# Performance work log

Measured on AMD Instinct MI355X. Metric: run time of the kernel, lower is better.

## Reference

```python
import jax, jax.numpy as jnp
import numpy as np

N, L, D, V, M = 64, 77, 768, 8, 8   # text batch, context_length, width, visual tokens, visual batch
H, LAYERS, VOCAB, E = 12, 12, 49409, 768
SOV, EOT = 49408, 49407  # splice-point token, end-of-text token


def setup_inputs() -> dict:
    rng = np.random.default_rng(0)
    text = rng.integers(1, 49400, size=(N, L))
    pos_y = rng.integers(1, 11, size=N)                      # splice position per sample
    eot = np.minimum(pos_y + rng.integers(5, 31, size=N), L - V)
    text[np.arange(N), pos_y] = SOV
    text[np.arange(N), eot] = EOT

    key = jax.random.key(0)
    ks = jax.random.split(key, 16)
    attn_std = D ** -0.5
    proj_std = (D ** -0.5) * ((2 * LAYERS) ** -0.5)
    fc_std = (2 * D) ** -0.5
    return {
        'text': jnp.asarray(text, jnp.int32),
        'visual_feature': jax.random.normal(ks[0], (M, V, D), jnp.float32),
        'tok_emb': jax.random.normal(ks[1], (VOCAB, D), jnp.float32) * 0.02,
        'pos_emb': jax.random.normal(ks[2], (L, D), jnp.float32) * 0.01,
        'ln1_w': jnp.ones((LAYERS, D), jnp.float32), 'ln1_b': jnp.zeros((LAYERS, D), jnp.float32),
        'in_w': jax.random.normal(ks[3], (LAYERS, 3 * D, D), jnp.float32) * attn_std,
        'in_b': jnp.zeros((LAYERS, 3 * D), jnp.float32),
        'out_w': jax.random.normal(ks[4], (LAYERS, D, D), jnp.float32) * proj_std,
        'out_b': jnp.zeros((LAYERS, D), jnp.float32),
        'ln2_w': jnp.ones((LAYERS, D), jnp.float32), 'ln2_b': jnp.zeros((LAYERS, D), jnp.float32),
        'fc_w': jax.random.normal(ks[5], (LAYERS, 4 * D, D), jnp.float32) * fc_std,
        'fc_b': jnp.zeros((LAYERS, 4 * D), jnp.float32),
        'pj_w': jax.random.normal(ks[6], (LAYERS, D, 4 * D), jnp.float32) * proj_std,
        'pj_b': jnp.zeros((LAYERS, D), jnp.float32),
        'lnf_w': jnp.ones((D,), jnp.float32), 'lnf_b': jnp.zeros((D,), jnp.float32),
        'text_proj': jax.random.normal(ks[7], (D, E), jnp.float32) * attn_std,
    }


def _layer_norm(x, w, b, eps=1e-5):
    mu = x.mean(-1, keepdims=True)
    var = ((x - mu) ** 2).mean(-1, keepdims=True)
    return (x - mu) * jax.lax.rsqrt(var + eps) * w + b


def reference(text, visual_feature, tok_emb, pos_emb, ln1_w, ln1_b, in_w, in_b,
              out_w, out_b, ln2_w, ln2_b, fc_w, fc_b, pj_w, pj_b, lnf_w, lnf_b, text_proj):
    text = text.astype(jnp.int32)
    pos_y = jnp.argmax(text == SOV, axis=1)        # [N] per-sample splice point
    eot = jnp.argmax(text == EOT, axis=1)          # [N]
    x = tok_emb[text]                              # [N,L,D]
    p = jnp.arange(L)[None, :]                     # [1,L]
    # fused gather replacing the torch.cat double loop:
    # out[p] = x[p] for p<pos_y ; visual[p-pos_y] for pos_y<=p<pos_y+V ; x[p-V+1] after
    src = jnp.clip(jnp.where(p < pos_y[:, None], p, p - V + 1), 0, L - 1)   # [N,L]
    xg = jnp.take_along_axis(x, src[..., None], axis=1)                      # [N,L,D]
    vis_mask = (p >= pos_y[:, None]) & (p < pos_y[:, None] + V)              # [N,L]
    vis_idx = jnp.clip(p - pos_y[:, None], 0, V - 1)                         # [N,L]
    vis = visual_feature[:, vis_idx]                                         # [M,N,L,D]
    h = jnp.where(vis_mask[None, :, :, None], vis, xg[None]) + pos_emb       # [M,N,L,D]
    h = h.reshape(M * N, L, D)

    mask = jnp.triu(jnp.full((L, L), -jnp.inf, jnp.float32), k=1)            # causal
    hd = D // H
    scale = 1.0 / np.sqrt(hd).astype(np.float32)
    for l in range(LAYERS):
        y = _layer_norm(h, ln1_w[l], ln1_b[l])
        qkv = y @ in_w[l].T + in_b[l]                                        # [B,L,3D]
        q, k, v = jnp.split(qkv, 3, axis=-1)
        sp = lambda t: t.reshape(-1, L, H, hd).transpose(0, 2, 1, 3)
        q, k, v = sp(q), sp(k), sp(v)
        att = jax.nn.softmax(jnp.einsum('bhqd,bhkd->bhqk', q, k) * scale + mask, axis=-1)
        o = jnp.einsum('bhqk,bhkd->bhqd', att, v).transpose(0, 2, 1, 3).reshape(-1, L, D)
        h = h + o @ out_w[l].T + out_b[l]
        y = _layer_norm(h, ln2_w[l], ln2_b[l]) @ fc_w[l].T + fc_b[l]
        y = y * jax.nn.sigmoid(1.702 * y)                                    # QuickGELU
        h = h + y @ pj_w[l].T + pj_b[l]

    h = _layer_norm(h, lnf_w, lnf_b).reshape(M, N, L, D)
    feats = h[:, jnp.arange(N), eot + V - 1] @ text_proj                     # [M,N,E]
    feats = feats / jnp.linalg.norm(feats, axis=-1, keepdims=True)
    feats = feats.mean(axis=1, keepdims=True)                                # [M,1,E]
    feats = feats / jnp.linalg.norm(feats, axis=-1, keepdims=True)
    return feats
```

## Files before the change

kernel.cpp:

```cpp
#include <hip/hip_runtime.h>


typedef short short8 __attribute__((ext_vector_type(8)));
typedef float floatx4 __attribute__((ext_vector_type(4)));
typedef unsigned int uint4v __attribute__((ext_vector_type(4)));
typedef unsigned short ushort4v __attribute__((ext_vector_type(4)));

#define SOV_TOK 49408
#define EOT_TOK 49407
#define ROWS 39424

__device__ __forceinline__ unsigned short f2bf(float f) {
  union { float f; unsigned int u; } v; v.f = f;
  return (unsigned short)((v.u + 0x7fffu + ((v.u >> 16) & 1u)) >> 16);
}

typedef const __attribute__((address_space(1))) void* gptr_t;
typedef __attribute__((address_space(3))) void* lptr_t;
__device__ __forceinline__ void glds16(const void* g, void* l) {
  __builtin_amdgcn_global_load_lds((gptr_t)g, (lptr_t)l, 16, 0, 0);
}

__device__ __forceinline__ float blockReduceSum256(float v, float* red) {
  __syncthreads();
  #pragma unroll
  for (int off = 32; off; off >>= 1) v += __shfl_down(v, off, 64);
  int wave = threadIdx.x >> 6, lane = threadIdx.x & 63;
  if (lane == 0) red[wave] = v;
  __syncthreads();
  return red[0] + red[1] + red[2] + red[3];
}

__global__ void idx_kernel(const int* text, int* posy, int* eot) {
  int n = threadIdx.x;
  int py = 0, et = 0; bool fp = false, fe = false;
  for (int j = 0; j < 77; j++) {
    int v = text[n * 77 + j];
    if (!fp && v == SOV_TOK) { py = j; fp = true; }
    if (!fe && v == EOT_TOK) { et = j; fe = true; }
  }
  posy[n] = py; eot[n] = et;
}

__global__ void cvt_kernel(const float* src, unsigned short* dst, int n) {
  int i = (blockIdx.x * 256 + threadIdx.x) * 4;
  if (i < n) {
    float4 v = *(const float4*)(src + i);
    ushort4v o;
    o.x = f2bf(v.x); o.y = f2bf(v.y); o.z = f2bf(v.z); o.w = f2bf(v.w);
    *(ushort4v*)(dst + i) = o;
  }
}

__global__ void transT_kernel(const float* tp, unsigned short* wt) {
  int id = blockIdx.x * 256 + threadIdx.x;
  int d = id / 768, e = id % 768;
  wt[(size_t)e * 768 + d] = f2bf(tp[id]);
}

__global__ void embed_kernel(const int* text, const float* vis,
                             const float* tok_emb, const float* pos_emb,
                             const int* posy, float* h) {
  int bp = blockIdx.x;
  int b = bp / 77, p = bp % 77;
  int mm = b >> 6, n = b & 63;
  int py = posy[n];
  int t = threadIdx.x;
  const float* srcp;
  if (p >= py && p < py + 8) {
    srcp = vis + ((size_t)mm * 8 + (p - py)) * 768;
  } else {
    int src = (p < py) ? p : p - 7;
    src = src < 0 ? 0 : (src > 76 ? 76 : src);
    int tok = text[n * 77 + src];
    srcp = tok_emb + (size_t)tok * 768;
  }
  float4 v = *(const float4*)(srcp + t * 4);
  float4 pe = *(const float4*)(pos_emb + (size_t)p * 768 + t * 4);
  v.x += pe.x; v.y += pe.y; v.z += pe.z; v.w += pe.w;
  *(float4*)(h + (size_t)bp * 768 + t * 4) = v;
}

__device__ __forceinline__ void ln_row(const float* xr, const float* w,
                                       const float* b, unsigned short* yr,
                                       float* red) {
  int t = threadIdx.x;
  float v0 = xr[t], v1 = xr[t + 256], v2 = xr[t + 512];
  float s = blockReduceSum256(v0 + v1 + v2, red);
  float mu = s * (1.f / 768.f);
  float d0 = v0 - mu, d1 = v1 - mu, d2 = v2 - mu;
  float q = blockReduceSum256(d0 * d0 + d1 * d1 + d2 * d2, red);
  float rstd = rsqrtf(q * (1.f / 768.f) + 1e-5f);
  yr[t]       = f2bf(d0 * rstd * w[t]       + b[t]);
  yr[t + 256] = f2bf(d1 * rstd * w[t + 256] + b[t + 256]);
  yr[t + 512] = f2bf(d2 * rstd * w[t + 512] + b[t + 512]);
}

__global__ void ln_kernel(const float* x, const float* w, const float* b,
                          unsigned short* y) {
  __shared__ float red[4];
  size_t r = blockIdx.x;
  ln_row(x + r * 768, w, b, y + r * 768, red);
}

__global__ void gather_ln_kernel(const float* h, const int* eot,
                                 const float* w, const float* b,
                                 unsigned short* y) {
  __shared__ float red[4];
  int r = blockIdx.x;
  int n = r & 63;
  size_t row = (size_t)r * 77 + (eot[n] + 7);
  ln_row(h + row * 768, w, b, y + (size_t)r * 768, red);
}

template <int MODE>
__global__ __launch_bounds__(512, 2)
void gemm256_kernel(const unsigned short* __restrict__ A,
                    const unsigned short* __restrict__ W,
                    const float* __restrict__ bias, void* __restrict__ outp,
                    const float* __restrict__ resid, int K, int cols) {
  __shared__ __align__(16) union LDSU {
    struct { unsigned short As[2][16384]; unsigned short Bs[2][16384]; } m;
    float ep[8][4352];
  } u;

  const int gx = gridDim.x;
  const int G = gx * gridDim.y;
  const int P = blockIdx.y * gx + blockIdx.x;
  const int q8 = G >> 3, r8 = G & 7;
  const int xcd = P & 7, ord = P >> 3;
  const int Lid =
      (xcd < r8 ? xcd * (q8 + 1) : r8 * (q8 + 1) + (xcd - r8) * q8) + ord;
  const int col0 = (Lid % gx) * 256;
  const int row0 = (Lid / gx) * 256;

  const int t = threadIdx.x;
  const int wave = t >> 6, lane = t & 63;
  const int m = lane & 15, quad = lane >> 4;
  const int wm = wave >> 2, wn = wave & 3;

  const int lr0 = t >> 3;
  const int cbe = ((t & 7) << 3) ^ ((lr0 & 7) << 3);
  const unsigned short* Abase = A + (size_t)(row0 + lr0) * K + cbe;
  const int grB0 = (lr0 & 31) + ((lr0 >> 5) << 6);
  const unsigned short* Bbase = W + (size_t)(col0 + grB0) * K + cbe;

#define STAGE_A(b, h, kb) {                                                  \
    const unsigned short* _p = Abase + (size_t)(h) * 64 * K + (kb);          \
    glds16(_p, &u.m.As[b][(h) * 8192 + wave * 512]);                         \
    glds16(_p + (size_t)128 * K, &u.m.As[b][(h) * 8192 + 4096 + wave * 512]); }
#define STAGE_B(b, h, kb) {                                                  \
    const unsigned short* _p = Bbase + (size_t)(h) * 32 * K + (kb);          \
    glds16(_p, &u.m.Bs[b][(h) * 8192 + wave * 512]);                         \
    glds16(_p + (size_t)128 * K, &u.m.Bs[b][(h) * 8192 + 4096 + wave * 512]); }

  const int aRow = wm * 64 + m;
  const int bRow = wn * 32 + m;
  const int sw = (m & 7) << 3;
  short8 af[4][2], bfr[2][2];
  floatx4 acc[8][4] = {};

#define RD_A(b, ha) {                                                        \
    _Pragma("unroll") for (int fi = 0; fi < 4; ++fi)                         \
    _Pragma("unroll") for (int ks = 0; ks < 2; ++ks)                         \
      af[fi][ks] = *(const short8*)&u.m.As[b][((ha) * 128 + aRow + fi * 16) * 64 \
                                          + (((ks << 5) | (quad << 3)) ^ sw)]; }
#define RD_B(b, hb) {                                                        \
    _Pragma("unroll") for (int fj = 0; fj < 2; ++fj)                         \
    _Pragma("unroll") for (int ks = 0; ks < 2; ++ks)                         \
      bfr[fj][ks] = *(const short8*)&u.m.Bs[b][((hb) * 128 + bRow + fj * 16) * 64\
                                          + (((ks << 5) | (quad << 3)) ^ sw)]; }
#define MFMA16(AH, BH) {                                                     \
    __builtin_amdgcn_s_setprio(1);                                           \
    _Pragma("unroll") for (int fi = 0; fi < 4; ++fi)                         \
    _Pragma("unroll") for (int fj = 0; fj < 2; ++fj)                         \
    _Pragma("unroll") for (int ks = 0; ks < 2; ++ks)                         \
      acc[(AH) * 4 + fi][(BH) * 2 + fj] =                                    \
          __builtin_amdgcn_mfma_f32_16x16x32_bf16(                           \
              af[fi][ks], bfr[fj][ks], acc[(AH) * 4 + fi][(BH) * 2 + fj],    \
              0, 0, 0);                                                      \
    __builtin_amdgcn_s_setprio(0); }
#define SBZ() __builtin_amdgcn_sched_barrier(0)
#define BAR() { SBZ(); __builtin_amdgcn_s_barrier(); SBZ(); }
#define WLDS() { asm volatile("s_waitcnt lgkmcnt(0)" ::: "memory"); SBZ(); }
#define WVM6() { asm volatile("s_waitcnt vmcnt(6)" ::: "memory"); SBZ(); }

  const int NT = K >> 6;
  const int NI = NT >> 1;

  STAGE_A(0, 0, 0); STAGE_A(0, 1, 0); STAGE_B(0, 0, 0); STAGE_B(0, 1, 0);
  STAGE_A(1, 0, 64); STAGE_B(1, 1, 64); STAGE_A(1, 1, 64);
  WVM6();
  BAR();

  for (int i = 0; i < NI; ++i) {
    const int T = i << 1;
    const int k1 = (T + 1) << 6;
    const int k2 = (T + 2 < NT ? T + 2 : NT - 1) << 6;
    const int k3 = (T + 3 < NT ? T + 3 : NT - 1) << 6;
    RD_A(0, 0); RD_B(0, 0); STAGE_B(1, 0, k1);
    BAR(); WLDS(); MFMA16(0, 0); BAR();
    RD_B(0, 1); STAGE_A(0, 0, k2);
    BAR(); WLDS(); MFMA16(0, 1); BAR();
    RD_A(0, 1); STAGE_B(0, 1, k2);
    BAR(); WLDS(); MFMA16(1, 1); BAR();
    RD_B(0, 0); STAGE_A(0, 1, k2); WVM6();
    BAR(); WLDS(); MFMA16(1, 0); BAR();
    RD_A(1, 0); RD_B(1, 0); STAGE_B(0, 0, k2);
    BAR(); WLDS(); MFMA16(0, 0); BAR();
    RD_B(1, 1); STAGE_A(1, 0, k3);
    BAR(); WLDS(); MFMA16(0, 1); BAR();
    RD_A(1, 1); STAGE_B(1, 1, k3);
    BAR(); WLDS(); MFMA16(1, 1); BAR();
    RD_B(1, 0); STAGE_A(1, 1, k3); WVM6();
    BAR(); WLDS(); MFMA16(1, 0); BAR();
  }
  asm volatile("s_waitcnt vmcnt(0)" ::: "memory");
  BAR();

  float* Ep = &u.ep[wave][0];
  const int g = lane >> 4, c4 = lane & 15;
  float bi[4];
  #pragma unroll
  for (int fj = 0; fj < 4; ++fj)
    bi[fj] = bias ? bias[col0 + wn * 64 + fj * 16 + m] : 0.f;

  #pragma unroll
  for (int h = 0; h < 2; ++h) {
    #pragma unroll
    for (int fi2 = 0; fi2 < 4; ++fi2) {
      #pragma unroll
      for (int fj = 0; fj < 4; ++fj) {
        #pragma unroll
        for (int reg = 0; reg < 4; ++reg) {
          float v = acc[h * 4 + fi2][fj][reg] + bi[fj];
          if (MODE == 1) v = v / (1.f + __expf(-1.702f * v));
          const int row_l = fi2 * 16 + quad * 4 + reg;
          Ep[row_l * 68 + ((fj * 16 + m) ^ (reg << 4))] = v;
        }
      }
    }
    asm volatile("s_waitcnt lgkmcnt(0)" ::: "memory");
    SBZ();
    #pragma unroll
    for (int tt = 0; tt < 16; ++tt) {
      const int row_l = tt * 4 + g;
      const float4 vv =
          *(const float4*)&Ep[row_l * 68 + ((c4 * 4) ^ (g << 4))];
      const size_t grow = (size_t)(row0 + wm * 128 + h * 64 + row_l);
      const size_t idx = grow * cols + (col0 + wn * 64 + c4 * 4);
      if (MODE == 0 || MODE == 1) {
        ushort4v o;
        o.x = f2bf(vv.x); o.y = f2bf(vv.y);
        o.z = f2bf(vv.z); o.w = f2bf(vv.w);
        *(ushort4v*)((unsigned short*)outp + idx) = o;
      } else if (MODE == 2) {
        const float4 r = *(const float4*)(resid + idx);
        float4 ov;
        ov.x = vv.x + r.x; ov.y = vv.y + r.y;
        ov.z = vv.z + r.z; ov.w = vv.w + r.w;
        *(float4*)((float*)outp + idx) = ov;
      } else {
        *(float4*)((float*)outp + idx) = vv;
      }
    }
  }
#undef STAGE_A
#undef STAGE_B
#undef RD_A
#undef RD_B
#undef MFMA16
#undef SBZ
#undef BAR
#undef WLDS
#undef WVM6
}

__global__ __launch_bounds__(256)
void attn_kernel(const unsigned short* qkv, unsigned short* o) {
  __shared__ __align__(16) union U {
    struct { unsigned short Qs[80 * 64]; unsigned short Ks[80 * 64]; } qk;
    unsigned short Ps[80 * 96];
  } u;
  __shared__ __align__(16) unsigned short Vt[64 * 96];
  __shared__ float S[80 * 81];

  int b = blockIdx.x, hh = blockIdx.y;
  int t = threadIdx.x, wave = t >> 6, lane = t & 63;
  int m = lane & 15, quad = lane >> 4;
  const unsigned short* base = qkv + (size_t)b * 77 * 2304 + hh * 64;

  for (int c = t; c < 640; c += 256) {
    int l = c >> 3, kc = (c & 7) * 8;
    uint4v q = {0, 0, 0, 0}, k = {0, 0, 0, 0};
    if (l < 77) {
      q = *(const uint4v*)(base + (size_t)l * 2304 + kc);
      k = *(const uint4v*)(base + (size_t)l * 2304 + 768 + kc);
    }
    *(uint4v*)(u.qk.Qs + l * 64 + kc) = q;
    *(uint4v*)(u.qk.Ks + l * 64 + kc) = k;
  }
  for (int c = t; c < 768; c += 256) {
    int l = c >> 3, d0 = (c & 7) * 8;
    union { uint4v v; unsigned short s[8]; } vv;
    vv.v = (uint4v){0, 0, 0, 0};
    if (l < 77) vv.v = *(const uint4v*)(base + (size_t)l * 2304 + 1536 + d0);
    #pragma unroll
    for (int j = 0; j < 8; j++) Vt[(d0 + j) * 96 + l] = vv.s[j];
  }
  __syncthreads();

  for (int idx = wave; idx < 15; idx += 4) {
    int ti = 0, a2 = 0;
    while (a2 + ti + 1 <= idx) { a2 += ti + 1; ti++; }
    int tj = idx - a2;
    floatx4 sa = {};
    #pragma unroll
    for (int k0 = 0; k0 < 64; k0 += 32) {
      short8 aq = *(const short8*)(u.qk.Qs + (ti * 16 + m) * 64 + k0 + quad * 8);
      short8 bk = *(const short8*)(u.qk.Ks + (tj * 16 + m) * 64 + k0 + quad * 8);
      sa = __builtin_amdgcn_mfma_f32_16x16x32_bf16(aq, bk, sa, 0, 0, 0);
    }
    #pragma unroll
    for (int r = 0; r < 4; r++)
      S[(ti * 16 + quad * 4 + r) * 81 + tj * 16 + m] = sa[r];
  }
  __syncthreads();

  if (t < 80) {
    int r = t;
    if (r < 77) {
      float mx = -1e30f;
      for (int j = 0; j <= r; j++) mx = fmaxf(mx, S[r * 81 + j]);
      float sum = 0.f;
      for (int j = 0; j <= r; j++) {
        float e = __expf((S[r * 81 + j] - mx) * 0.125f);
        S[r * 81 + j] = e; sum += e;
      }
      float inv = 1.f / sum;
      for (int j = 0; j < 96; j++)
        u.Ps[r * 96 + j] = (j <= r) ? f2bf(S[r * 81 + j] * inv) : (unsigned short)0;
    } else {
      for (int j = 0; j < 96; j++) u.Ps[r * 96 + j] = 0;
    }
  }
  __syncthreads();

  for (int idx = wave; idx < 20; idx += 4) {
    int ti = idx >> 2, tj = idx & 3;
    floatx4 oa = {};
    #pragma unroll
    for (int k0 = 0; k0 < 96; k0 += 32) {
      short8 ap = *(const short8*)(u.Ps + (ti * 16 + m) * 96 + k0 + quad * 8);
      short8 bv = *(const short8*)(Vt + (tj * 16 + m) * 96 + k0 + quad * 8);
      oa = __builtin_amdgcn_mfma_f32_16x16x32_bf16(ap, bv, oa, 0, 0, 0);
    }
    #pragma unroll
    for (int r = 0; r < 4; r++) {
      int l = ti * 16 + quad * 4 + r;
      if (l < 77)
        o[((size_t)b * 77 + l) * 768 + hh * 64 + tj * 16 + m] = f2bf(oa[r]);
    }
  }
}

__global__ void reduce_kernel(const float* feats, float* out) {
  __shared__ float red[4];
  int mfig = blockIdx.x;
  int t = threadIdx.x;
  float a0 = 0.f, a1 = 0.f, a2 = 0.f;
  for (int n = 0; n < 64; n++) {
    const float* fr = feats + ((size_t)mfig * 64 + n) * 768;
    float v0 = fr[t], v1 = fr[t + 256], v2 = fr[t + 512];
    float q = blockReduceSum256(v0 * v0 + v1 * v1 + v2 * v2, red);
    float rn = rsqrtf(q);
    a0 += v0 * rn; a1 += v1 * rn; a2 += v2 * rn;
  }
  float q = blockReduceSum256(a0 * a0 + a1 * a1 + a2 * a2, red);
  float rn = rsqrtf(q);
  out[mfig * 768 + t]       = a0 * rn;
  out[mfig * 768 + t + 256] = a1 * rn;
  out[mfig * 768 + t + 512] = a2 * rn;
}

extern "C" void kernel_launch(void* const* d_in, const int* in_sizes, int n_in,
                              void* d_out, int out_size, void* d_ws,
                              size_t ws_size, hipStream_t stream) {
  (void)in_sizes; (void)n_in; (void)out_size; (void)ws_size;
  const int*   text      = (const int*)d_in[0];
  const float* visf      = (const float*)d_in[1];
  const float* tok_emb   = (const float*)d_in[2];
  const float* pos_emb   = (const float*)d_in[3];
  const float* ln1_w     = (const float*)d_in[4];
  const float* ln1_b     = (const float*)d_in[5];
  const float* in_w      = (const float*)d_in[6];
  const float* in_b      = (const float*)d_in[7];
  const float* out_w     = (const float*)d_in[8];
  const float* out_b     = (const float*)d_in[9];
  const float* ln2_w     = (const float*)d_in[10];
  const float* ln2_b     = (const float*)d_in[11];
  const float* fc_w      = (const float*)d_in[12];
  const float* fc_b      = (const float*)d_in[13];
  const float* pj_w      = (const float*)d_in[14];
  const float* pj_b      = (const float*)d_in[15];
  const float* lnf_w     = (const float*)d_in[16];
  const float* lnf_b     = (const float*)d_in[17];
  const float* text_proj = (const float*)d_in[18];
  float* out = (float*)d_out;

  char* p = (char*)d_ws;
  auto alloc = [&](size_t bytes) {
    char* q = p; p += (bytes + 255) & ~(size_t)255; return q;
  };
  int* posy = (int*)alloc(64 * 4);
  int* eot  = (int*)alloc(64 * 4);
  float* h            = (float*)alloc((size_t)ROWS * 768 * 4);
  unsigned short* y   = (unsigned short*)alloc((size_t)ROWS * 768 * 2);
  unsigned short* qkv = (unsigned short*)alloc((size_t)ROWS * 2304 * 2);
  unsigned short* ob  = (unsigned short*)alloc((size_t)ROWS * 768 * 2);
  unsigned short* act = qkv;
  unsigned short* wqkv = (unsigned short*)alloc((size_t)2304 * 768 * 2);
  unsigned short* wout = (unsigned short*)alloc((size_t)768 * 768 * 2);
  unsigned short* wfc  = (unsigned short*)alloc((size_t)3072 * 768 * 2);
  unsigned short* wpj  = (unsigned short*)alloc((size_t)768 * 3072 * 2);
  unsigned short* wt   = (unsigned short*)alloc((size_t)768 * 768 * 2);
  unsigned short* afin = (unsigned short*)alloc((size_t)512 * 768 * 2);
  float* feats = (float*)alloc((size_t)512 * 768 * 4);

  idx_kernel<<<1, 64, 0, stream>>>(text, posy, eot);
  transT_kernel<<<(768 * 768) / 256, 256, 0, stream>>>(text_proj, wt);
  embed_kernel<<<ROWS, 192, 0, stream>>>(text, visf, tok_emb, pos_emb, posy, h);

  const int NQKV = 2304 * 768, NOUT = 768 * 768, NFC = 3072 * 768;
  for (int l = 0; l < 12; l++) {
    cvt_kernel<<<NQKV / 1024, 256, 0, stream>>>(in_w + (size_t)l * NQKV, wqkv, NQKV);
    cvt_kernel<<<NOUT / 1024, 256, 0, stream>>>(out_w + (size_t)l * NOUT, wout, NOUT);
    cvt_kernel<<<NFC / 1024, 256, 0, stream>>>(fc_w + (size_t)l * NFC, wfc, NFC);
    cvt_kernel<<<NFC / 1024, 256, 0, stream>>>(pj_w + (size_t)l * NFC, wpj, NFC);

    ln_kernel<<<ROWS, 256, 0, stream>>>(h, ln1_w + l * 768, ln1_b + l * 768, y);
    gemm256_kernel<0><<<dim3(9, 154), 512, 0, stream>>>(
        y, wqkv, in_b + l * 2304, qkv, nullptr, 768, 2304);
    attn_kernel<<<dim3(512, 12), 256, 0, stream>>>(qkv, ob);
    gemm256_kernel<2><<<dim3(3, 154), 512, 0, stream>>>(
        ob, wout, out_b + l * 768, h, h, 768, 768);
    ln_kernel<<<ROWS, 256, 0, stream>>>(h, ln2_w + l * 768, ln2_b + l * 768, y);
    gemm256_kernel<1><<<dim3(12, 154), 512, 0, stream>>>(
        y, wfc, fc_b + l * 3072, act, nullptr, 768, 3072);
    gemm256_kernel<2><<<dim3(3, 154), 512, 0, stream>>>(
        act, wpj, pj_b + l * 768, h, h, 3072, 768);
  }

  gather_ln_kernel<<<512, 256, 0, stream>>>(h, eot, lnf_w, lnf_b, afin);
  gemm256_kernel<3><<<dim3(3, 2), 512, 0, stream>>>(
      afin, wt, nullptr, feats, nullptr, 768, 768);
  reduce_kernel<<<8, 256, 0, stream>>>(feats, out);
}
```

Before: 12.30 ms.

## Fuse weight conversions, use wave-per-row layernorm, peel GEMM tail, packed bf16 stores

```diff
diff --git a/kernel.cpp b/kernel.cpp
--- a/kernel.cpp
+++ b/kernel.cpp
@@ -13,6 +13,12 @@
 __device__ __forceinline__ unsigned short f2bf(float f) {
   union { float f; unsigned int u; } v; v.f = f;
   return (unsigned short)((v.u + 0x7fffu + ((v.u >> 16) & 1u)) >> 16);
+}
+
+__device__ __forceinline__ unsigned int pk_bf16(float a, float b) {
+  unsigned int r;
+  asm("v_cvt_pk_bf16_f32 %0, %1, %2" : "=v"(r) : "v"(a), "v"(b));
+  return r;
 }
 
 typedef const __attribute__((address_space(1))) void* gptr_t;
@@ -42,14 +48,21 @@
   posy[n] = py; eot[n] = et;
 }
 
-__global__ void cvt_kernel(const float* src, unsigned short* dst, int n) {
+__global__ __launch_bounds__(256)
+void cvt4_kernel(const float* __restrict__ w0, const float* __restrict__ w1,
+                 const float* __restrict__ w2, const float* __restrict__ w3,
+                 unsigned short* __restrict__ d0, unsigned short* __restrict__ d1,
+                 unsigned short* __restrict__ d2, unsigned short* __restrict__ d3) {
+  const int NQKV = 2304 * 768, NOUT = 768 * 768, NFC = 3072 * 768;
   int i = (blockIdx.x * 256 + threadIdx.x) * 4;
-  if (i < n) {
-    float4 v = *(const float4*)(src + i);
-    ushort4v o;
-    o.x = f2bf(v.x); o.y = f2bf(v.y); o.z = f2bf(v.z); o.w = f2bf(v.w);
-    *(ushort4v*)(dst + i) = o;
-  }
+  const float* s; unsigned short* d;
+  if (i < NQKV)                    { s = w0 + i;  d = d0 + i; }
+  else if (i < NQKV + NOUT)        { int j = i - NQKV; s = w1 + j; d = d1 + j; }
+  else if (i < NQKV + NOUT + NFC)  { int j = i - NQKV - NOUT; s = w2 + j; d = d2 + j; }
+  else                             { int j = i - NQKV - NOUT - NFC; s = w3 + j; d = d3 + j; }
+  float4 v = *(const float4*)s;
+  uint2 o; o.x = pk_bf16(v.x, v.y); o.y = pk_bf16(v.z, v.w);
+  *(uint2*)d = o;
 }
 
 __global__ void transT_kernel(const float* tp, unsigned short* wt) {
@@ -81,26 +94,46 @@
   *(float4*)(h + (size_t)bp * 768 + t * 4) = v;
 }
 
-__device__ __forceinline__ void ln_row(const float* xr, const float* w,
-                                       const float* b, unsigned short* yr,
-                                       float* red) {
-  int t = threadIdx.x;
-  float v0 = xr[t], v1 = xr[t + 256], v2 = xr[t + 512];
-  float s = blockReduceSum256(v0 + v1 + v2, red);
-  float mu = s * (1.f / 768.f);
-  float d0 = v0 - mu, d1 = v1 - mu, d2 = v2 - mu;
-  float q = blockReduceSum256(d0 * d0 + d1 * d1 + d2 * d2, red);
-  float rstd = rsqrtf(q * (1.f / 768.f) + 1e-5f);
-  yr[t]       = f2bf(d0 * rstd * w[t]       + b[t]);
-  yr[t + 256] = f2bf(d1 * rstd * w[t + 256] + b[t + 256]);
-  yr[t + 512] = f2bf(d2 * rstd * w[t + 512] + b[t + 512]);
-}
-
-__global__ void ln_kernel(const float* x, const float* w, const float* b,
-                          unsigned short* y) {
-  __shared__ float red[4];
-  size_t r = blockIdx.x;
-  ln_row(x + r * 768, w, b, y + r * 768, red);
+__global__ __launch_bounds__(256)
+void ln4_kernel(const float* __restrict__ x, const float* __restrict__ w,
+                const float* __restrict__ b, unsigned short* __restrict__ y) {
+  const int wave = threadIdx.x >> 6, lane = threadIdx.x & 63;
+  const size_t r = (size_t)blockIdx.x * 4 + wave;
+  const float* xr = x + r * 768;
+  const int c = lane * 4;
+  const float4 v0 = *(const float4*)(xr + c);
+  const float4 v1 = *(const float4*)(xr + 256 + c);
+  const float4 v2 = *(const float4*)(xr + 512 + c);
+  float s = v0.x + v0.y + v0.z + v0.w + v1.x + v1.y + v1.z + v1.w +
+            v2.x + v2.y + v2.z + v2.w;
+  #pragma unroll
+  for (int off = 32; off; off >>= 1) s += __shfl_xor(s, off, 64);
+  const float mu = s * (1.f / 768.f);
+  const float d0 = v0.x - mu, d1 = v0.y - mu, d2 = v0.z - mu, d3 = v0.w - mu;
+  const float d4 = v1.x - mu, d5 = v1.y - mu, d6 = v1.z - mu, d7 = v1.w - mu;
+  const float d8 = v2.x - mu, d9 = v2.y - mu, d10 = v2.z - mu, d11 = v2.w - mu;
+  float q = d0 * d0 + d1 * d1 + d2 * d2 + d3 * d3 + d4 * d4 + d5 * d5 +
+            d6 * d6 + d7 * d7 + d8 * d8 + d9 * d9 + d10 * d10 + d11 * d11;
+  #pragma unroll
+  for (int off = 32; off; off >>= 1) q += __shfl_xor(q, off, 64);
+  const float rstd = rsqrtf(q * (1.f / 768.f) + 1e-5f);
+  const float4 w0 = *(const float4*)(w + c);
+  const float4 w1 = *(const float4*)(w + 256 + c);
+  const float4 w2 = *(const float4*)(w + 512 + c);
+  const float4 b0 = *(const float4*)(b + c);
+  const float4 b1 = *(const float4*)(b + 256 + c);
+  const float4 b2 = *(const float4*)(b + 512 + c);
+  unsigned short* yr = y + r * 768;
+  uint2 o;
+  o.x = pk_bf16(d0 * rstd * w0.x + b0.x, d1 * rstd * w0.y + b0.y);
+  o.y = pk_bf16(d2 * rstd * w0.z + b0.z, d3 * rstd * w0.w + b0.w);
+  *(uint2*)(yr + c) = o;
+  o.x = pk_bf16(d4 * rstd * w1.x + b1.x, d5 * rstd * w1.y + b1.y);
+  o.y = pk_bf16(d6 * rstd * w1.z + b1.z, d7 * rstd * w1.w + b1.w);
+  *(uint2*)(yr + 256 + c) = o;
+  o.x = pk_bf16(d8 * rstd * w2.x + b2.x, d9 * rstd * w2.y + b2.y);
+  o.y = pk_bf16(d10 * rstd * w2.z + b2.z, d11 * rstd * w2.w + b2.w);
+  *(uint2*)(yr + 512 + c) = o;
 }
 
 __global__ void gather_ln_kernel(const float* h, const int* eot,
@@ -110,7 +143,18 @@
   int r = blockIdx.x;
   int n = r & 63;
   size_t row = (size_t)r * 77 + (eot[n] + 7);
-  ln_row(h + row * 768, w, b, y + (size_t)r * 768, red);
+  const float* xr = h + row * 768;
+  int t = threadIdx.x;
+  float v0 = xr[t], v1 = xr[t + 256], v2 = xr[t + 512];
+  float s = blockReduceSum256(v0 + v1 + v2, red);
+  float mu = s * (1.f / 768.f);
+  float e0 = v0 - mu, e1 = v1 - mu, e2 = v2 - mu;
+  float q = blockReduceSum256(e0 * e0 + e1 * e1 + e2 * e2, red);
+  float rstd = rsqrtf(q * (1.f / 768.f) + 1e-5f);
+  unsigned short* yr = y + (size_t)r * 768;
+  yr[t]       = f2bf(e0 * rstd * w[t]       + b[t]);
+  yr[t + 256] = f2bf(e1 * rstd * w[t + 256] + b[t + 256]);
+  yr[t + 512] = f2bf(e2 * rstd * w[t + 512] + b[t + 512]);
 }
 
 template <int MODE>
@@ -184,6 +228,7 @@
 #define BAR() { SBZ(); __builtin_amdgcn_s_barrier(); SBZ(); }
 #define WLDS() { asm volatile("s_waitcnt lgkmcnt(0)" ::: "memory"); SBZ(); }
 #define WVM6() { asm volatile("s_waitcnt vmcnt(6)" ::: "memory"); SBZ(); }
+#define WVM0() { asm volatile("s_waitcnt vmcnt(0)" ::: "memory"); SBZ(); }
 
   const int NT = K >> 6;
   const int NI = NT >> 1;
@@ -193,11 +238,11 @@
   WVM6();
   BAR();
 
-  for (int i = 0; i < NI; ++i) {
+  for (int i = 0; i < NI - 1; ++i) {
     const int T = i << 1;
     const int k1 = (T + 1) << 6;
-    const int k2 = (T + 2 < NT ? T + 2 : NT - 1) << 6;
-    const int k3 = (T + 3 < NT ? T + 3 : NT - 1) << 6;
+    const int k2 = (T + 2) << 6;
+    const int k3 = (T + 3) << 6;
     RD_A(0, 0); RD_B(0, 0); STAGE_B(1, 0, k1);
     BAR(); WLDS(); MFMA16(0, 0); BAR();
     RD_B(0, 1); STAGE_A(0, 0, k2);
@@ -215,8 +260,25 @@
     RD_B(1, 0); STAGE_A(1, 1, k3); WVM6();
     BAR(); WLDS(); MFMA16(1, 0); BAR();
   }
-  asm volatile("s_waitcnt vmcnt(0)" ::: "memory");
-  BAR();
+  {
+    const int k1 = (NT - 1) << 6;
+    RD_A(0, 0); RD_B(0, 0); STAGE_B(1, 0, k1);
+    BAR(); WLDS(); MFMA16(0, 0); BAR();
+    RD_B(0, 1);
+    BAR(); WLDS(); MFMA16(0, 1); BAR();
+    RD_A(0, 1);
+    BAR(); WLDS(); MFMA16(1, 1); BAR();
+    RD_B(0, 0); WVM0();
+    BAR(); WLDS(); MFMA16(1, 0); BAR();
+    RD_A(1, 0); RD_B(1, 0);
+    BAR(); WLDS(); MFMA16(0, 0); BAR();
+    RD_B(1, 1);
+    BAR(); WLDS(); MFMA16(0, 1); BAR();
+    RD_A(1, 1);
+    BAR(); WLDS(); MFMA16(1, 1); BAR();
+    RD_B(1, 0);
+    BAR(); WLDS(); MFMA16(1, 0); BAR();
+  }
 
   float* Ep = &u.ep[wave][0];
   const int g = lane >> 4, c4 = lane & 15;
@@ -234,7 +296,8 @@
         #pragma unroll
         for (int reg = 0; reg < 4; ++reg) {
           float v = acc[h * 4 + fi2][fj][reg] + bi[fj];
-          if (MODE == 1) v = v / (1.f + __expf(-1.702f * v));
+          if (MODE == 1)
+            v = v * __builtin_amdgcn_rcpf(1.f + __expf(-1.702f * v));
           const int row_l = fi2 * 16 + quad * 4 + reg;
           Ep[row_l * 68 + ((fj * 16 + m) ^ (reg << 4))] = v;
         }
@@ -250,10 +313,10 @@
       const size_t grow = (size_t)(row0 + wm * 128 + h * 64 + row_l);
       const size_t idx = grow * cols + (col0 + wn * 64 + c4 * 4);
       if (MODE == 0 || MODE == 1) {
-        ushort4v o;
-        o.x = f2bf(vv.x); o.y = f2bf(vv.y);
-        o.z = f2bf(vv.z); o.w = f2bf(vv.w);
-        *(ushort4v*)((unsigned short*)outp + idx) = o;
+        uint2 o;
+        o.x = pk_bf16(vv.x, vv.y);
+        o.y = pk_bf16(vv.z, vv.w);
+        *(uint2*)((unsigned short*)outp + idx) = o;
       } else if (MODE == 2) {
         const float4 r = *(const float4*)(resid + idx);
         float4 ov;
@@ -274,6 +337,7 @@
 #undef BAR
 #undef WLDS
 #undef WVM6
+#undef WVM0
 }
 
 __global__ __launch_bounds__(256)
@@ -432,19 +496,22 @@
   embed_kernel<<<ROWS, 192, 0, stream>>>(text, visf, tok_emb, pos_emb, posy, h);
 
   const int NQKV = 2304 * 768, NOUT = 768 * 768, NFC = 3072 * 768;
+  const int CVT_BLKS = (NQKV + NOUT + 2 * NFC) / 1024;
   for (int l = 0; l < 12; l++) {
-    cvt_kernel<<<NQKV / 1024, 256, 0, stream>>>(in_w + (size_t)l * NQKV, wqkv, NQKV);
-    cvt_kernel<<<NOUT / 1024, 256, 0, stream>>>(out_w + (size_t)l * NOUT, wout, NOUT);
-    cvt_kernel<<<NFC / 1024, 256, 0, stream>>>(fc_w + (size_t)l * NFC, wfc, NFC);
-    cvt_kernel<<<NFC / 1024, 256, 0, stream>>>(pj_w + (size_t)l * NFC, wpj, NFC);
-
-    ln_kernel<<<ROWS, 256, 0, stream>>>(h, ln1_w + l * 768, ln1_b + l * 768, y);
+    cvt4_kernel<<<CVT_BLKS, 256, 0, stream>>>(
+        in_w + (size_t)l * NQKV, out_w + (size_t)l * NOUT,
+        fc_w + (size_t)l * NFC, pj_w + (size_t)l * NFC,
+        wqkv, wout, wfc, wpj);
+
+    ln4_kernel<<<ROWS / 4, 256, 0, stream>>>(h, ln1_w + l * 768,
+                                             ln1_b + l * 768, y);
     gemm256_kernel<0><<<dim3(9, 154), 512, 0, stream>>>(
         y, wqkv, in_b + l * 2304, qkv, nullptr, 768, 2304);
     attn_kernel<<<dim3(512, 12), 256, 0, stream>>>(qkv, ob);
     gemm256_kernel<2><<<dim3(3, 154), 512, 0, stream>>>(
         ob, wout, out_b + l * 768, h, h, 768, 768);
-    ln_kernel<<<ROWS, 256, 0, stream>>>(h, ln2_w + l * 768, ln2_b + l * 768, y);
+    ln4_kernel<<<ROWS / 4, 256, 0, stream>>>(h, ln2_w + l * 768,
+                                             ln2_b + l * 768, y);
     gemm256_kernel<1><<<dim3(12, 154), 512, 0, stream>>>(
         y, wfc, fc_b + l * 3072, act, nullptr, 768, 3072);
     gemm256_kernel<2><<<dim3(3, 154), 512, 0, stream>>>(
```

New measurement: 11.63 ms. 5.5% less time.
